# Kernel optimization log

Hardware: AMD Instinct MI355X
Metric: run time of the kernel (lower is better)

The kernel has to match this reference:

```python
import jax, jax.numpy as jnp
import numpy as np

N = 1_000_000      # total points
G = 256            # number of interaction clusters (segments)
D_IN = 4           # [energy, x, y, z] per-point features
H1, H2, LATENT = 64, 128, 256
D_OUT = 3          # vertex position dims


def setup_inputs() -> dict:
    key = jax.random.key(0)
    ks = jax.random.split(key, 10)
    point_cloud = jax.random.normal(ks[0], (N, 5), dtype=jnp.float32)
    seg_ids = jnp.sort(jax.random.randint(ks[1], (N,), 0, G, dtype=jnp.int64))
    def lin(k, fan_in, fan_out):
        s = 1.0 / np.sqrt(fan_in)
        return jax.random.uniform(k, (fan_in, fan_out), jnp.float32, -s, s)
    W1 = lin(ks[2], D_IN, H1);   b1 = jnp.zeros((H1,), jnp.float32)
    W2 = lin(ks[3], H1, H2);     b2 = jnp.zeros((H2,), jnp.float32)
    W3 = lin(ks[4], H2, LATENT); b3 = jnp.zeros((LATENT,), jnp.float32)
    Wf = lin(ks[5], LATENT, D_OUT); bf = jnp.zeros((D_OUT,), jnp.float32)
    return {"point_cloud": point_cloud, "W1": W1, "b1": b1, "W2": W2, "b2": b2,
            "W3": W3, "b3": b3, "Wf": Wf, "bf": bf, "seg_ids": seg_ids}


def reference(point_cloud, W1, b1, W2, b2, W3, b3, Wf, bf, seg_ids):
    pos = point_cloud[:, 1:4]          # [N,3]
    x = point_cloud[:, 4:5]            # [N,1] energy
    # --- per-segment centroids (segment mean, single pass) ---
    counts = jax.ops.segment_sum(jnp.ones((pos.shape[0],), pos.dtype), seg_ids,
                                 num_segments=G)                      # [G]
    centroids = jax.ops.segment_sum(pos, seg_ids, num_segments=G)
    centroids = centroids / jnp.maximum(counts, 1.0)[:, None]         # [G,3]
    # --- PointNet encoder: shared per-point MLP + per-segment max-pool ---
    feats = jnp.concatenate([x, pos], axis=1)                         # [N,4]
    h = jax.nn.relu(feats @ W1 + b1)                                  # [N,64]
    h = jax.nn.relu(h @ W2 + b2)                                      # [N,128]
    h = h @ W3 + b3                                                   # [N,256]
    pooled = jax.ops.segment_max(h, seg_ids, num_segments=G)          # [G,256]
    # --- final Linear + Softplus head, added to centroids ---
    out = jax.nn.softplus(pooled @ Wf + bf)                           # [G,3]
    return centroids + out
```

## Files before the change

kernel.cpp:

```cpp
#include <hip/hip_runtime.h>
#include <float.h>

typedef __bf16 bf16x8 __attribute__((ext_vector_type(8)));
typedef __bf16 bf16x4 __attribute__((ext_vector_type(4)));
typedef float  f32x4  __attribute__((ext_vector_type(4)));

#define G      256
#define MT     32
#define H1DIM  64
#define H2DIM  128
#define LAT    256
#define H1PAD  72
#define H2PAD  136

__device__ __forceinline__ unsigned mapf(float f) {
  unsigned u = __float_as_uint(f);
  return (u & 0x80000000u) ? ~u : (u | 0x80000000u);
}
__device__ __forceinline__ float unmapf(unsigned u) {
  return (u & 0x80000000u) ? __uint_as_float(u & 0x7fffffffu) : __uint_as_float(~u);
}

__device__ __forceinline__ void flush2(f32x4 v0, f32x4 v1,
                                       int s, int w, int q, int nn,
                                       const float* __restrict__ b3,
                                       unsigned* __restrict__ pooled) {
  f32x4 vv[2] = {v0, v1};
  #pragma unroll
  for (int mt = 0; mt < 2; ++mt)
    #pragma unroll
    for (int r = 0; r < 4; ++r) {
      int feat = w * 32 + mt * 16 + q * 4 + r;
      float v = vv[mt][r] + b3[feat];
      v = fmaxf(v, __shfl_xor(v, 1));
      v = fmaxf(v, __shfl_xor(v, 2));
      v = fmaxf(v, __shfl_xor(v, 4));
      v = fmaxf(v, __shfl_xor(v, 8));
      if (nn == 0) atomicMax(&pooled[s * LAT + feat], mapf(v));
    }
}

__global__ __launch_bounds__(512, 4) void mlp_kernel(
    const float* __restrict__ pc,
    const float* __restrict__ W1, const float* __restrict__ b1,
    const float* __restrict__ W2, const float* __restrict__ b2,
    const float* __restrict__ W3, const float* __restrict__ b3,
    const int* __restrict__ sid,
    unsigned* __restrict__ pooled,
    float* __restrict__ sums,
    int n, int tiles_per_block) {
  __shared__ __align__(16) __bf16 shF[MT][8];
  __shared__ __align__(16) __bf16 sh1[MT][H1PAD];
  __shared__ __align__(16) __bf16 sh2[MT][H2PAD];
  __shared__ int segt[MT];

  const int t  = threadIdx.x;
  const int w  = t >> 6;
  const int lane = t & 63;
  const int q  = lane >> 4;
  const int nn = lane & 15;

  bf16x8 w1f = {};
  float b1r[4] = {0.f, 0.f, 0.f, 0.f};
  if (w >= 4) {
    int wl = w - 4;
    #pragma unroll
    for (int j = 0; j < 8; ++j) {
      int k = q * 8 + j;
      w1f[j] = (k < 4) ? (__bf16)W1[k * H1DIM + wl * 16 + nn] : (__bf16)0.f;
    }
    #pragma unroll
    for (int r = 0; r < 4; ++r) b1r[r] = b1[wl * 16 + q * 4 + r];
  }

  bf16x8 w2f[2];
  float  b2r[4];
  {
    int m = w * 16 + nn;
    #pragma unroll
    for (int ks = 0; ks < 2; ++ks)
      #pragma unroll
      for (int j = 0; j < 8; ++j)
        w2f[ks][j] = (__bf16)W2[(ks * 32 + q * 8 + j) * H2DIM + m];
    #pragma unroll
    for (int r = 0; r < 4; ++r) b2r[r] = b2[w * 16 + q * 4 + r];
  }

  bf16x8 w3f[2][4];
  #pragma unroll
  for (int mt = 0; mt < 2; ++mt) {
    int m = w * 32 + mt * 16 + nn;
    #pragma unroll
    for (int ks = 0; ks < 4; ++ks)
      #pragma unroll
      for (int j = 0; j < 8; ++j)
        w3f[mt][ks][j] = (__bf16)W3[(ks * 32 + q * 8 + j) * LAT + m];
  }

  const f32x4 zero4 = {0.f, 0.f, 0.f, 0.f};
  const bf16x8 zero8 = {};
  const f32x4 neginf4 = {-FLT_MAX, -FLT_MAX, -FLT_MAX, -FLT_MAX};

  f32x4 run[2];
  run[0] = neginf4; run[1] = neginf4;

  float cx = 0.f, cy = 0.f, cz = 0.f, cc = 0.f;
  int   cseg = -1;

  const int tile0 = blockIdx.x * tiles_per_block;
  int first = tile0 * MT; if (first > n - 1) first = n - 1;
  int s_cur = sid[first];

  float pf1 = 0.f, pf2 = 0.f, pf3 = 0.f, pfx = 0.f;
  int   pfs = 0; bool pfv = false;
  if (t < MT) {
    int p = tile0 * MT + t;
    pfv = p < n;
    int pcl = pfv ? p : (n - 1);
    const float* pp = pc + (size_t)pcl * 5;
    pf1 = pp[1]; pf2 = pp[2]; pf3 = pp[3]; pfx = pp[4];
    pfs = sid[pcl];
  }

  for (int ti = 0; ti < tiles_per_block; ++ti) {
    const int base = (tile0 + ti) * MT;
    if (base >= n) break;

    if (t < MT) {
      bf16x8 v = {};
      v[0] = (__bf16)pfx;
      v[1] = (__bf16)pf1;
      v[2] = (__bf16)pf2;
      v[3] = (__bf16)pf3;
      *reinterpret_cast<bf16x8*>(&shF[t][0]) = v;
      segt[t] = pfs;
      if (pfv) {
        if (pfs != cseg) {
          if (cc > 0.f) {
            atomicAdd(&sums[cseg * 4 + 0], cx);
            atomicAdd(&sums[cseg * 4 + 1], cy);
            atomicAdd(&sums[cseg * 4 + 2], cz);
            atomicAdd(&sums[cseg * 4 + 3], cc);
          }
          cseg = pfs; cx = 0.f; cy = 0.f; cz = 0.f; cc = 0.f;
        }
        cx += pf1; cy += pf2; cz += pf3; cc += 1.f;
      }
    }
    __syncthreads();

    if (t < MT) {
      int p = (tile0 + ti + 1) * MT + t;
      pfv = p < n;
      int pcl = pfv ? p : (n - 1);
      const float* pp = pc + (size_t)pcl * 5;
      pf1 = pp[1]; pf2 = pp[2]; pf3 = pp[3]; pfx = pp[4];
      pfs = sid[pcl];
    }

    if (w >= 4) {
      int wl = w - 4;
      f32x4 acc1[2];
      #pragma unroll
      for (int nt = 0; nt < 2; ++nt) {
        bf16x8 ld = *reinterpret_cast<const bf16x8*>(&shF[nt * 16 + nn][0]);
        bf16x8 af = (q == 0) ? ld : zero8;
        acc1[nt] = __builtin_amdgcn_mfma_f32_16x16x32_bf16(w1f, af, zero4, 0, 0, 0);
      }
      #pragma unroll
      for (int nt = 0; nt < 2; ++nt) {
        bf16x4 pk;
        #pragma unroll
        for (int r = 0; r < 4; ++r)
          pk[r] = (__bf16)fmaxf(acc1[nt][r] + b1r[r], 0.f);
        *reinterpret_cast<bf16x4*>(&sh1[nt * 16 + nn][wl * 16 + q * 4]) = pk;
      }
    }
    __syncthreads();

    {
      f32x4 acc2[2];
      acc2[0] = zero4; acc2[1] = zero4;
      #pragma unroll
      for (int ks = 0; ks < 2; ++ks) {
        bf16x8 bfr[2];
        #pragma unroll
        for (int nt = 0; nt < 2; ++nt)
          bfr[nt] = *reinterpret_cast<const bf16x8*>(&sh1[nt * 16 + nn][ks * 32 + q * 8]);
        #pragma unroll
        for (int nt = 0; nt < 2; ++nt)
          acc2[nt] = __builtin_amdgcn_mfma_f32_16x16x32_bf16(w2f[ks], bfr[nt], acc2[nt], 0, 0, 0);
      }
      #pragma unroll
      for (int nt = 0; nt < 2; ++nt) {
        bf16x4 pk;
        #pragma unroll
        for (int r = 0; r < 4; ++r)
          pk[r] = (__bf16)fmaxf(acc2[nt][r] + b2r[r], 0.f);
        *reinterpret_cast<bf16x4*>(&sh2[nt * 16 + nn][w * 16 + q * 4]) = pk;
      }
    }
    __syncthreads();

    f32x4 acc3[2][2];
    #pragma unroll
    for (int mt = 0; mt < 2; ++mt)
      #pragma unroll
      for (int nt = 0; nt < 2; ++nt) acc3[mt][nt] = zero4;
    #pragma unroll
    for (int ks = 0; ks < 4; ++ks) {
      bf16x8 bfr[2];
      #pragma unroll
      for (int nt = 0; nt < 2; ++nt)
        bfr[nt] = *reinterpret_cast<const bf16x8*>(&sh2[nt * 16 + nn][ks * 32 + q * 8]);
      #pragma unroll
      for (int mt = 0; mt < 2; ++mt)
        #pragma unroll
        for (int nt = 0; nt < 2; ++nt)
          acc3[mt][nt] = __builtin_amdgcn_mfma_f32_16x16x32_bf16(w3f[mt][ks], bfr[nt], acc3[mt][nt], 0, 0, 0);
    }

    int smin = segt[0], smax = segt[MT - 1];
    if (smin != s_cur) {
      flush2(run[0], run[1], s_cur, w, q, nn, b3, pooled);
      run[0] = neginf4; run[1] = neginf4;
      s_cur = smin;
    }
    if (smin == smax) {
      #pragma unroll
      for (int mt = 0; mt < 2; ++mt)
        #pragma unroll
        for (int r = 0; r < 4; ++r)
          run[mt][r] = fmaxf(run[mt][r], fmaxf(acc3[mt][0][r], acc3[mt][1][r]));
    } else {
      int sg0 = segt[nn], sg1 = segt[16 + nn];
      for (int s = smin; s <= smax; ++s) {
        f32x4 tmp[2];
        #pragma unroll
        for (int mt = 0; mt < 2; ++mt)
          #pragma unroll
          for (int r = 0; r < 4; ++r) {
            float v0 = (sg0 == s) ? acc3[mt][0][r] : -FLT_MAX;
            float v1 = (sg1 == s) ? acc3[mt][1][r] : -FLT_MAX;
            tmp[mt][r] = fmaxf(v0, v1);
          }
        if (s < smax) {
          if (s == s_cur) {
            #pragma unroll
            for (int mt = 0; mt < 2; ++mt)
              #pragma unroll
              for (int r = 0; r < 4; ++r) run[mt][r] = fmaxf(run[mt][r], tmp[mt][r]);
            flush2(run[0], run[1], s, w, q, nn, b3, pooled);
            run[0] = neginf4; run[1] = neginf4;
          } else {
            flush2(tmp[0], tmp[1], s, w, q, nn, b3, pooled);
          }
        } else {
          #pragma unroll
          for (int mt = 0; mt < 2; ++mt)
            #pragma unroll
            for (int r = 0; r < 4; ++r) run[mt][r] = fmaxf(run[mt][r], tmp[mt][r]);
        }
      }
      s_cur = smax;
    }
    __syncthreads();
  }
  flush2(run[0], run[1], s_cur, w, q, nn, b3, pooled);

  if (t < MT && cc > 0.f) {
    atomicAdd(&sums[cseg * 4 + 0], cx);
    atomicAdd(&sums[cseg * 4 + 1], cy);
    atomicAdd(&sums[cseg * 4 + 2], cz);
    atomicAdd(&sums[cseg * 4 + 3], cc);
  }
}

__global__ void final_kernel(const float* __restrict__ sums, const unsigned* __restrict__ pooled,
                             const float* __restrict__ Wf, const float* __restrict__ bfv,
                             float* __restrict__ out) {
  __shared__ float red[4][3];
  int g = blockIdx.x;
  int t = threadIdx.x;
  unsigned u = pooled[g * LAT + t];
  float f = u ? unmapf(u) : 0.f;
  float s0 = f * Wf[t * 3 + 0];
  float s1 = f * Wf[t * 3 + 1];
  float s2 = f * Wf[t * 3 + 2];
  #pragma unroll
  for (int off = 1; off < 64; off <<= 1) {
    s0 += __shfl_xor(s0, off);
    s1 += __shfl_xor(s1, off);
    s2 += __shfl_xor(s2, off);
  }
  int wave = t >> 6;
  if ((t & 63) == 0) { red[wave][0] = s0; red[wave][1] = s1; red[wave][2] = s2; }
  __syncthreads();
  if (t < 3) {
    float acc = bfv[t] + red[0][t] + red[1][t] + red[2][t] + red[3][t];
    float sp  = fmaxf(acc, 0.f) + log1pf(expf(-fabsf(acc)));
    float cnt = fmaxf(sums[g * 4 + 3], 1.f);
    float cen = sums[g * 4 + t] / cnt;
    out[g * 3 + t] = cen + sp;
  }
}

extern "C" void kernel_launch(void* const* d_in, const int* in_sizes, int n_in,
                              void* d_out, int out_size, void* d_ws, size_t ws_size,
                              hipStream_t stream) {
  const float* pc  = (const float*)d_in[0];
  const float* W1  = (const float*)d_in[1];
  const float* b1  = (const float*)d_in[2];
  const float* W2  = (const float*)d_in[3];
  const float* b2  = (const float*)d_in[4];
  const float* W3  = (const float*)d_in[5];
  const float* b3  = (const float*)d_in[6];
  const float* Wf  = (const float*)d_in[7];
  const float* bfv = (const float*)d_in[8];
  const int*   sid = (const int*)d_in[9];
  int n = in_sizes[0] / 5;

  float*    sums   = (float*)d_ws;
  unsigned* pooled = (unsigned*)((char*)d_ws + 4096);
  hipMemsetAsync(d_ws, 0, 4096 + (size_t)G * LAT * 4, stream);

  int tiles   = (n + MT - 1) / MT;
  int nblocks = 512;
  int tpb     = (tiles + nblocks - 1) / nblocks;
  mlp_kernel<<<nblocks, 512, 0, stream>>>(pc, W1, b1, W2, b2, W3, b3, sid, pooled, sums, n, tpb);

  final_kernel<<<G, 256, 0, stream>>>(sums, pooled, Wf, bfv, (float*)d_out);
}
```

Baseline: 222.1 us.

## Make each wave process its own point tile independently, weights in LDS

Restructures the MLP kernel so each wave owns a contiguous chunk of 16-point tiles and runs all three layers on its own. This removes the block-wide __syncthreads between layers. W2 and W3 fragments are pre-swizzled into shared memory once per block instead of living in registers, and b1 is folded into the first MFMA via a constant-1 input. Each wave now holds 16 running-max accumulators for the full 256-wide latent. The cost is more LDS traffic for weight fragments, higher register pressure (launch bounds occupancy lowered to 2), and half as many blocks.

```diff
diff --git a/kernel.cpp b/kernel.cpp
--- a/kernel.cpp
+++ b/kernel.cpp
@@ -6,12 +6,12 @@
 typedef float  f32x4  __attribute__((ext_vector_type(4)));
 
 #define G      256
-#define MT     32
+#define NPT    16
+#define NW     8
 #define H1DIM  64
 #define H2DIM  128
 #define LAT    256
-#define H1PAD  72
-#define H2PAD  136
+#define A2PAD  136
 
 __device__ __forceinline__ unsigned mapf(float f) {
   unsigned u = __float_as_uint(f);
@@ -21,26 +21,22 @@
   return (u & 0x80000000u) ? __uint_as_float(u & 0x7fffffffu) : __uint_as_float(~u);
 }
 
-__device__ __forceinline__ void flush2(f32x4 v0, f32x4 v1,
-                                       int s, int w, int q, int nn,
-                                       const float* __restrict__ b3,
-                                       unsigned* __restrict__ pooled) {
-  f32x4 vv[2] = {v0, v1};
-  #pragma unroll
-  for (int mt = 0; mt < 2; ++mt)
-    #pragma unroll
-    for (int r = 0; r < 4; ++r) {
-      int feat = w * 32 + mt * 16 + q * 4 + r;
-      float v = vv[mt][r] + b3[feat];
-      v = fmaxf(v, __shfl_xor(v, 1));
-      v = fmaxf(v, __shfl_xor(v, 2));
-      v = fmaxf(v, __shfl_xor(v, 4));
-      v = fmaxf(v, __shfl_xor(v, 8));
-      if (nn == 0) atomicMax(&pooled[s * LAT + feat], mapf(v));
-    }
-}
-
-__global__ __launch_bounds__(512, 4) void mlp_kernel(
+__device__ __forceinline__ void flush_mt(f32x4 v4, int mt, int s, int q, int nn,
+                                         const float* __restrict__ b3,
+                                         unsigned* __restrict__ pooled) {
+  #pragma unroll
+  for (int r = 0; r < 4; ++r) {
+    int feat = mt * 16 + q * 4 + r;
+    float v = v4[r] + b3[feat];
+    v = fmaxf(v, __shfl_xor(v, 1));
+    v = fmaxf(v, __shfl_xor(v, 2));
+    v = fmaxf(v, __shfl_xor(v, 4));
+    v = fmaxf(v, __shfl_xor(v, 8));
+    if (nn == 0) atomicMax(&pooled[s * LAT + feat], mapf(v));
+  }
+}
+
+__global__ __launch_bounds__(512, 2) void mlp_kernel(
     const float* __restrict__ pc,
     const float* __restrict__ W1, const float* __restrict__ b1,
     const float* __restrict__ W2, const float* __restrict__ b2,
@@ -48,73 +44,73 @@
     const int* __restrict__ sid,
     unsigned* __restrict__ pooled,
     float* __restrict__ sums,
-    int n, int tiles_per_block) {
-  __shared__ __align__(16) __bf16 shF[MT][8];
-  __shared__ __align__(16) __bf16 sh1[MT][H1PAD];
-  __shared__ __align__(16) __bf16 sh2[MT][H2PAD];
-  __shared__ int segt[MT];
-
-  const int t  = threadIdx.x;
-  const int w  = t >> 6;
+    int n, int tiles_per_wave) {
+  __shared__ bf16x8 w2lds[H2DIM / 16 * 2 * 64];
+  __shared__ bf16x8 w3lds[LAT / 16 * 4 * 64];
+  __shared__ __align__(16) float b2lds[H2DIM];
+  __shared__ __align__(16) __bf16 act[NW][NPT][A2PAD];
+
+  const int t    = threadIdx.x;
+  const int w    = t >> 6;
   const int lane = t & 63;
-  const int q  = lane >> 4;
-  const int nn = lane & 15;
-
-  bf16x8 w1f = {};
-  float b1r[4] = {0.f, 0.f, 0.f, 0.f};
-  if (w >= 4) {
-    int wl = w - 4;
+  const int q    = lane >> 4;
+  const int nn   = lane & 15;
+
+  for (int idx = t; idx < LAT / 16 * 4 * 64; idx += 512) {
+    int mt = idx >> 8, ks = (idx >> 6) & 3, l = idx & 63;
+    int lq = l >> 4, lm = (mt << 4) + (l & 15);
+    bf16x8 v;
+    #pragma unroll
+    for (int j = 0; j < 8; ++j)
+      v[j] = (__bf16)W3[(ks * 32 + lq * 8 + j) * LAT + lm];
+    w3lds[idx] = v;
+  }
+  for (int idx = t; idx < H2DIM / 16 * 2 * 64; idx += 512) {
+    int mt = idx >> 7, ks = (idx >> 6) & 1, l = idx & 63;
+    int lq = l >> 4, lm = (mt << 4) + (l & 15);
+    bf16x8 v;
+    #pragma unroll
+    for (int j = 0; j < 8; ++j)
+      v[j] = (__bf16)W2[(ks * 32 + lq * 8 + j) * H2DIM + lm];
+    w2lds[idx] = v;
+  }
+  if (t < H2DIM) b2lds[t] = b2[t];
+
+  bf16x8 w1r[4];
+  #pragma unroll
+  for (int mt = 0; mt < 4; ++mt)
     #pragma unroll
     for (int j = 0; j < 8; ++j) {
       int k = q * 8 + j;
-      w1f[j] = (k < 4) ? (__bf16)W1[k * H1DIM + wl * 16 + nn] : (__bf16)0.f;
-    }
-    #pragma unroll
-    for (int r = 0; r < 4; ++r) b1r[r] = b1[wl * 16 + q * 4 + r];
-  }
-
-  bf16x8 w2f[2];
-  float  b2r[4];
-  {
-    int m = w * 16 + nn;
-    #pragma unroll
-    for (int ks = 0; ks < 2; ++ks)
-      #pragma unroll
-      for (int j = 0; j < 8; ++j)
-        w2f[ks][j] = (__bf16)W2[(ks * 32 + q * 8 + j) * H2DIM + m];
-    #pragma unroll
-    for (int r = 0; r < 4; ++r) b2r[r] = b2[w * 16 + q * 4 + r];
-  }
-
-  bf16x8 w3f[2][4];
-  #pragma unroll
-  for (int mt = 0; mt < 2; ++mt) {
-    int m = w * 32 + mt * 16 + nn;
-    #pragma unroll
-    for (int ks = 0; ks < 4; ++ks)
-      #pragma unroll
-      for (int j = 0; j < 8; ++j)
-        w3f[mt][ks][j] = (__bf16)W3[(ks * 32 + q * 8 + j) * LAT + m];
-  }
-
-  const f32x4 zero4 = {0.f, 0.f, 0.f, 0.f};
+      float v = 0.f;
+      if (k < 4)       v = W1[k * H1DIM + mt * 16 + nn];
+      else if (k == 4) v = b1[mt * 16 + nn];
+      w1r[mt][j] = (__bf16)v;
+    }
+
+  __syncthreads();
+
+  const int gw = blockIdx.x * NW + w;
+  const int chunk_base = gw * tiles_per_wave * NPT;
+  if (chunk_base >= n) return;
+
+  const f32x4  zero4 = {0.f, 0.f, 0.f, 0.f};
   const bf16x8 zero8 = {};
-  const f32x4 neginf4 = {-FLT_MAX, -FLT_MAX, -FLT_MAX, -FLT_MAX};
-
-  f32x4 run[2];
-  run[0] = neginf4; run[1] = neginf4;
+
+  f32x4 run[16];
+  #pragma unroll
+  for (int mt = 0; mt < 16; ++mt)
+    run[mt] = (f32x4){-FLT_MAX, -FLT_MAX, -FLT_MAX, -FLT_MAX};
 
   float cx = 0.f, cy = 0.f, cz = 0.f, cc = 0.f;
   int   cseg = -1;
 
-  const int tile0 = blockIdx.x * tiles_per_block;
-  int first = tile0 * MT; if (first > n - 1) first = n - 1;
-  int s_cur = sid[first];
+  int s_cur = sid[chunk_base];
 
   float pf1 = 0.f, pf2 = 0.f, pf3 = 0.f, pfx = 0.f;
-  int   pfs = 0; bool pfv = false;
-  if (t < MT) {
-    int p = tile0 * MT + t;
+  int pfs = 0; bool pfv = false;
+  if (q == 0) {
+    int p = chunk_base + nn;
     pfv = p < n;
     int pcl = pfv ? p : (n - 1);
     const float* pp = pc + (size_t)pcl * 5;
@@ -122,35 +118,14 @@
     pfs = sid[pcl];
   }
 
-  for (int ti = 0; ti < tiles_per_block; ++ti) {
-    const int base = (tile0 + ti) * MT;
+  for (int ti = 0; ti < tiles_per_wave; ++ti) {
+    const int base = chunk_base + ti * NPT;
     if (base >= n) break;
 
-    if (t < MT) {
-      bf16x8 v = {};
-      v[0] = (__bf16)pfx;
-      v[1] = (__bf16)pf1;
-      v[2] = (__bf16)pf2;
-      v[3] = (__bf16)pf3;
-      *reinterpret_cast<bf16x8*>(&shF[t][0]) = v;
-      segt[t] = pfs;
-      if (pfv) {
-        if (pfs != cseg) {
-          if (cc > 0.f) {
-            atomicAdd(&sums[cseg * 4 + 0], cx);
-            atomicAdd(&sums[cseg * 4 + 1], cy);
-            atomicAdd(&sums[cseg * 4 + 2], cz);
-            atomicAdd(&sums[cseg * 4 + 3], cc);
-          }
-          cseg = pfs; cx = 0.f; cy = 0.f; cz = 0.f; cc = 0.f;
-        }
-        cx += pf1; cy += pf2; cz += pf3; cc += 1.f;
-      }
-    }
-    __syncthreads();
-
-    if (t < MT) {
-      int p = (tile0 + ti + 1) * MT + t;
+    float c1 = pf1, c2 = pf2, c3 = pf3, cxv = pfx;
+    int csid = pfs; bool cval = pfv;
+    if (q == 0) {
+      int p = base + NPT + nn;
       pfv = p < n;
       int pcl = pfv ? p : (n - 1);
       const float* pp = pc + (size_t)pcl * 5;
@@ -158,117 +133,110 @@
       pfs = sid[pcl];
     }
 
-    if (w >= 4) {
-      int wl = w - 4;
-      f32x4 acc1[2];
+    if (q == 0 && cval) {
+      if (csid != cseg) {
+        if (cc > 0.f) {
+          atomicAdd(&sums[cseg * 4 + 0], cx);
+          atomicAdd(&sums[cseg * 4 + 1], cy);
+          atomicAdd(&sums[cseg * 4 + 2], cz);
+          atomicAdd(&sums[cseg * 4 + 3], cc);
+        }
+        cseg = csid; cx = 0.f; cy = 0.f; cz = 0.f; cc = 0.f;
+      }
+      cx += c1; cy += c2; cz += c3; cc += 1.f;
+    }
+
+    int sgl  = __shfl(csid, nn);
+    int smin = __builtin_amdgcn_readfirstlane(__shfl(csid, 0));
+    int smax = __builtin_amdgcn_readfirstlane(__shfl(csid, NPT - 1));
+
+    if (smin != s_cur) {
       #pragma unroll
-      for (int nt = 0; nt < 2; ++nt) {
-        bf16x8 ld = *reinterpret_cast<const bf16x8*>(&shF[nt * 16 + nn][0]);
-        bf16x8 af = (q == 0) ? ld : zero8;
-        acc1[nt] = __builtin_amdgcn_mfma_f32_16x16x32_bf16(w1f, af, zero4, 0, 0, 0);
+      for (int mt = 0; mt < 16; ++mt) {
+        flush_mt(run[mt], mt, s_cur, q, nn, b3, pooled);
+        run[mt] = (f32x4){-FLT_MAX, -FLT_MAX, -FLT_MAX, -FLT_MAX};
       }
+      s_cur = smin;
+    }
+    const int  s_before = s_cur;
+    const bool fast = (smin == smax);
+
+    bf16x8 bO = zero8;
+    if (q == 0) {
+      bO[0] = (__bf16)cxv;
+      bO[1] = (__bf16)c1;
+      bO[2] = (__bf16)c2;
+      bO[3] = (__bf16)c3;
+      bO[4] = (__bf16)1.0f;
+    }
+    #pragma unroll
+    for (int mt = 0; mt < 4; ++mt) {
+      f32x4 a = __builtin_amdgcn_mfma_f32_16x16x32_bf16(w1r[mt], bO, zero4, 0, 0, 0);
+      bf16x4 pk;
       #pragma unroll
-      for (int nt = 0; nt < 2; ++nt) {
-        bf16x4 pk;
+      for (int r = 0; r < 4; ++r) pk[r] = (__bf16)fmaxf(a[r], 0.f);
+      *reinterpret_cast<bf16x4*>(&act[w][nn][mt * 16 + q * 4]) = pk;
+    }
+
+    bf16x8 f2[2];
+    #pragma unroll
+    for (int ks = 0; ks < 2; ++ks)
+      f2[ks] = *reinterpret_cast<const bf16x8*>(&act[w][nn][ks * 32 + q * 8]);
+
+    #pragma unroll
+    for (int mt = 0; mt < 8; ++mt) {
+      f32x4 a = zero4;
+      a = __builtin_amdgcn_mfma_f32_16x16x32_bf16(w2lds[(mt * 2 + 0) * 64 + lane], f2[0], a, 0, 0, 0);
+      a = __builtin_amdgcn_mfma_f32_16x16x32_bf16(w2lds[(mt * 2 + 1) * 64 + lane], f2[1], a, 0, 0, 0);
+      f32x4 bb = *reinterpret_cast<const f32x4*>(&b2lds[mt * 16 + q * 4]);
+      bf16x4 pk;
+      #pragma unroll
+      for (int r = 0; r < 4; ++r) pk[r] = (__bf16)fmaxf(a[r] + bb[r], 0.f);
+      *reinterpret_cast<bf16x4*>(&act[w][nn][mt * 16 + q * 4]) = pk;
+    }
+
+    bf16x8 f3[4];
+    #pragma unroll
+    for (int ks = 0; ks < 4; ++ks)
+      f3[ks] = *reinterpret_cast<const bf16x8*>(&act[w][nn][ks * 32 + q * 8]);
+
+    #pragma unroll
+    for (int mt = 0; mt < 16; ++mt) {
+      f32x4 a = zero4;
+      #pragma unroll
+      for (int ks = 0; ks < 4; ++ks)
+        a = __builtin_amdgcn_mfma_f32_16x16x32_bf16(w3lds[(mt * 4 + ks) * 64 + lane], f3[ks], a, 0, 0, 0);
+      if (fast) {
         #pragma unroll
-        for (int r = 0; r < 4; ++r)
-          pk[r] = (__bf16)fmaxf(acc1[nt][r] + b1r[r], 0.f);
-        *reinterpret_cast<bf16x4*>(&sh1[nt * 16 + nn][wl * 16 + q * 4]) = pk;
-      }
-    }
-    __syncthreads();
-
-    {
-      f32x4 acc2[2];
-      acc2[0] = zero4; acc2[1] = zero4;
-      #pragma unroll
-      for (int ks = 0; ks < 2; ++ks) {
-        bf16x8 bfr[2];
-        #pragma unroll
-        for (int nt = 0; nt < 2; ++nt)
-          bfr[nt] = *reinterpret_cast<const bf16x8*>(&sh1[nt * 16 + nn][ks * 32 + q * 8]);
-        #pragma unroll
-        for (int nt = 0; nt < 2; ++nt)
-          acc2[nt] = __builtin_amdgcn_mfma_f32_16x16x32_bf16(w2f[ks], bfr[nt], acc2[nt], 0, 0, 0);
-      }
-      #pragma unroll
-      for (int nt = 0; nt < 2; ++nt) {
-        bf16x4 pk;
-        #pragma unroll
-        for (int r = 0; r < 4; ++r)
-          pk[r] = (__bf16)fmaxf(acc2[nt][r] + b2r[r], 0.f);
-        *reinterpret_cast<bf16x4*>(&sh2[nt * 16 + nn][w * 16 + q * 4]) = pk;
-      }
-    }
-    __syncthreads();
-
-    f32x4 acc3[2][2];
-    #pragma unroll
-    for (int mt = 0; mt < 2; ++mt)
-      #pragma unroll
-      for (int nt = 0; nt < 2; ++nt) acc3[mt][nt] = zero4;
-    #pragma unroll
-    for (int ks = 0; ks < 4; ++ks) {
-      bf16x8 bfr[2];
-      #pragma unroll
-      for (int nt = 0; nt < 2; ++nt)
-        bfr[nt] = *reinterpret_cast<const bf16x8*>(&sh2[nt * 16 + nn][ks * 32 + q * 8]);
-      #pragma unroll
-      for (int mt = 0; mt < 2; ++mt)
-        #pragma unroll
-        for (int nt = 0; nt < 2; ++nt)
-          acc3[mt][nt] = __builtin_amdgcn_mfma_f32_16x16x32_bf16(w3f[mt][ks], bfr[nt], acc3[mt][nt], 0, 0, 0);
-    }
-
-    int smin = segt[0], smax = segt[MT - 1];
-    if (smin != s_cur) {
-      flush2(run[0], run[1], s_cur, w, q, nn, b3, pooled);
-      run[0] = neginf4; run[1] = neginf4;
-      s_cur = smin;
-    }
-    if (smin == smax) {
-      #pragma unroll
-      for (int mt = 0; mt < 2; ++mt)
-        #pragma unroll
-        for (int r = 0; r < 4; ++r)
-          run[mt][r] = fmaxf(run[mt][r], fmaxf(acc3[mt][0][r], acc3[mt][1][r]));
-    } else {
-      int sg0 = segt[nn], sg1 = segt[16 + nn];
-      for (int s = smin; s <= smax; ++s) {
-        f32x4 tmp[2];
-        #pragma unroll
-        for (int mt = 0; mt < 2; ++mt)
+        for (int r = 0; r < 4; ++r) run[mt][r] = fmaxf(run[mt][r], a[r]);
+      } else {
+        for (int s = smin; s <= smax; ++s) {
+          f32x4 tmp;
           #pragma unroll
-          for (int r = 0; r < 4; ++r) {
-            float v0 = (sg0 == s) ? acc3[mt][0][r] : -FLT_MAX;
-            float v1 = (sg1 == s) ? acc3[mt][1][r] : -FLT_MAX;
-            tmp[mt][r] = fmaxf(v0, v1);
+          for (int r = 0; r < 4; ++r) tmp[r] = (sgl == s) ? a[r] : -FLT_MAX;
+          if (s < smax) {
+            if (s == s_before) {
+              #pragma unroll
+              for (int r = 0; r < 4; ++r) run[mt][r] = fmaxf(run[mt][r], tmp[r]);
+              flush_mt(run[mt], mt, s, q, nn, b3, pooled);
+              run[mt] = (f32x4){-FLT_MAX, -FLT_MAX, -FLT_MAX, -FLT_MAX};
+            } else {
+              flush_mt(tmp, mt, s, q, nn, b3, pooled);
+            }
+          } else {
+            #pragma unroll
+            for (int r = 0; r < 4; ++r) run[mt][r] = fmaxf(run[mt][r], tmp[r]);
           }
-        if (s < smax) {
-          if (s == s_cur) {
-            #pragma unroll
-            for (int mt = 0; mt < 2; ++mt)
-              #pragma unroll
-              for (int r = 0; r < 4; ++r) run[mt][r] = fmaxf(run[mt][r], tmp[mt][r]);
-            flush2(run[0], run[1], s, w, q, nn, b3, pooled);
-            run[0] = neginf4; run[1] = neginf4;
-          } else {
-            flush2(tmp[0], tmp[1], s, w, q, nn, b3, pooled);
-          }
-        } else {
-          #pragma unroll
-          for (int mt = 0; mt < 2; ++mt)
-            #pragma unroll
-            for (int r = 0; r < 4; ++r) run[mt][r] = fmaxf(run[mt][r], tmp[mt][r]);
         }
       }
-      s_cur = smax;
-    }
-    __syncthreads();
-  }
-  flush2(run[0], run[1], s_cur, w, q, nn, b3, pooled);
-
-  if (t < MT && cc > 0.f) {
+    }
+    if (!fast) s_cur = smax;
+  }
+
+  #pragma unroll
+  for (int mt = 0; mt < 16; ++mt)
+    flush_mt(run[mt], mt, s_cur, q, nn, b3, pooled);
+  if (q == 0 && cc > 0.f) {
     atomicAdd(&sums[cseg * 4 + 0], cx);
     atomicAdd(&sums[cseg * 4 + 1], cy);
     atomicAdd(&sums[cseg * 4 + 2], cz);
@@ -324,10 +292,11 @@
   unsigned* pooled = (unsigned*)((char*)d_ws + 4096);
   hipMemsetAsync(d_ws, 0, 4096 + (size_t)G * LAT * 4, stream);
 
-  int tiles   = (n + MT - 1) / MT;
-  int nblocks = 512;
-  int tpb     = (tiles + nblocks - 1) / nblocks;
-  mlp_kernel<<<nblocks, 512, 0, stream>>>(pc, W1, b1, W2, b2, W3, b3, sid, pooled, sums, n, tpb);
+  int tiles       = (n + NPT - 1) / NPT;
+  int nblocks     = 256;
+  int waves_total = nblocks * NW;
+  int tpw         = (tiles + waves_total - 1) / waves_total;
+  mlp_kernel<<<nblocks, 512, 0, stream>>>(pc, W1, b1, W2, b2, W3, b3, sid, pooled, sums, n, tpw);
 
   final_kernel<<<G, 256, 0, stream>>>(sums, pooled, Wf, bfv, (float*)d_out);
 }
```

Result: slower. 305.1 us (+37.4%).
